# Performance work log

Measured on AMD Instinct MI355X. Metric: run time of the kernel, lower is better.

The kernel has to match this reference:

```python
import jax, jax.numpy as jnp
import numpy as np

RATIO = 4

def positional_encoding(d_model, max_len, w_s):
    # w_s: (B,) per-example frequency warp. pe[b, p, 0::2]=sin, pe[b, p, 1::2]=cos
    pos = jnp.arange(max_len, dtype=jnp.float32)                      # (L,)
    div = jnp.power(10000.0, jnp.arange(0, d_model, 2, dtype=jnp.float32) / d_model)  # (d/2,)
    ang = w_s[:, None, None] * pos[None, :, None] / div[None, None, :]  # (B, L, d/2)
    pe = jnp.stack([jnp.sin(ang), jnp.cos(ang)], axis=-1)             # (B, L, d/2, 2)
    return pe.reshape(w_s.shape[0], max_len, d_model)

def setup_inputs() -> dict:
    key = jax.random.key(0)
    ks = jax.random.split(key, 6)
    B, Tds, L, D = 32, 2048, 512, 256
    q = jax.random.normal(ks[0], (B, Tds, D), dtype=jnp.float32)
    k = jax.random.normal(ks[1], (B, L, D), dtype=jnp.float32)
    v = jax.random.normal(ks[2], (B, L, D), dtype=jnp.float32)
    w_compress = jax.random.normal(ks[3], (D // RATIO, D), dtype=jnp.float32) * (D ** -0.5)
    text_lengths = jax.random.randint(ks[4], (B,), L // 2, L + 1).at[0].set(L)
    mel_lengths = jax.random.randint(ks[5], (B,), (Tds * RATIO) // 2, Tds * RATIO + 1).at[0].set(Tds * RATIO)
    return {"q": q, "k": k, "v": v, "w_compress": w_compress,
            "text_lengths": text_lengths, "mel_lengths": mel_lengths}

def reference(q, k, v, w_compress, text_lengths, mel_lengths):
    B, Tds, D = q.shape
    L = k.shape[1]
    # padding masks (True = padded)
    text_mask = jnp.arange(L)[None, :] >= text_lengths[:, None]            # (B, L)
    mel_mask_ds = jnp.arange(Tds)[None, :] >= (mel_lengths // RATIO)[:, None]  # (B, Tds)
    # positional encodings
    q = q + positional_encoding(D, Tds, jnp.ones((B,), dtype=jnp.float32))
    w_s = mel_lengths.astype(jnp.float32) / RATIO / text_lengths.astype(jnp.float32)
    k = k + positional_encoding(D, L, w_s)
    q = q * (float(D) ** -0.5)
    # scores + masked softmax over text axis
    scores = jnp.einsum('btd,bld->btl', q, k)                              # (B, Tds, L)
    scores = jnp.where(text_mask[:, None, :], -jnp.inf, scores)
    align = jax.nn.softmax(scores, axis=-1)
    align = jnp.where(mel_mask_ds[:, :, None], 0.0, align)
    # hard argmax one-hot, straight-through blend
    idx = jnp.argmax(align, axis=-1)                                       # (B, Tds)
    align_oh = jax.nn.one_hot(idx, L, dtype=align.dtype)
    align_oh = jnp.where(mel_mask_ds[:, :, None], 0.0, align_oh)
    blend = align + jax.lax.stop_gradient(align_oh - align)
    attn = jnp.einsum('btl,bld->btd', blend, v)                            # (B, Tds, D)
    # Compress (Linear D -> D//ratio, no bias) then transpose(1,2)
    out = jnp.einsum('btd,cd->bct', attn, w_compress)                      # (B, D//ratio, Tds)
    return out, align
```

## Files before the change

kernel.cpp:

```cpp
#include <hip/hip_runtime.h>
#include <math.h>

#define NB  32
#define TDS 2048
#define LL  512
#define DD  256
#define DC  64
#define GAP_THR 4e-4f

typedef __attribute__((ext_vector_type(8)))  short short8;
typedef __attribute__((ext_vector_type(16))) float f32x16;

__device__ __forceinline__ unsigned short f2bf(float x) {
    union { float f; unsigned u; } v; v.f = x;
    unsigned r = v.u + 0x7fffu + ((v.u >> 16) & 1u);
    return (unsigned short)(r >> 16);
}
__device__ __forceinline__ float bf2f(unsigned short h) {
    union { unsigned u; float f; } v; v.u = ((unsigned)h) << 16;
    return v.f;
}


__global__ void peq_kernel(float* __restrict__ peq, int* __restrict__ cnt) {
    int idx = blockIdx.x * 256 + threadIdx.x;
    if (idx == 0) cnt[0] = 0;
    int t = idx >> 8;
    int d = idx & 255;
    int i = d >> 1;
    double invdiv = exp((double)i * (-9.210340371976184 / 128.0));
    double ang = (double)t * invdiv;
    double s, c;
    sincos(ang, &s, &c);
    peq[idx] = (float)((d & 1) ? c : s);
}

__global__ __launch_bounds__(256)
void pek_kernel(const float* __restrict__ k,
                const int* __restrict__ text_lengths,
                const int* __restrict__ mel_lengths,
                char* __restrict__ kps) {
    __shared__ double invdiv[128];
    const int tid = threadIdx.x;
    if (tid < 128) invdiv[tid] = exp((double)tid * (-9.210340371976184 / 128.0));
    __syncthreads();
    int f = blockIdx.x * 256 + tid;
    int b = f >> 14;
    int r = f & 16383;
    int ks = r >> 11;
    int r2 = r & 2047;
    int cs = r2 >> 7;
    int r3 = r2 & 127;
    int kh = r3 >> 6;
    int g  = (r3 >> 5) & 1;
    int lane32 = r3 & 31;
    int l  = cs * 32 + lane32;
    int k0 = ks * 32 + kh * 16 + g * 8;
    const float* kr = k + ((size_t)(b * LL + l)) * DD + k0;
    float4 kv0 = *(const float4*)(kr);
    float4 kv1 = *(const float4*)(kr + 4);
    float kv[8] = {kv0.x, kv0.y, kv0.z, kv0.w, kv1.x, kv1.y, kv1.z, kv1.w};
    double wsd = ((double)mel_lengths[b] * 0.25) / (double)text_lengths[b];
    double base_ang = wsd * (double)l;
    unsigned short h[8], lo8[8];
#pragma unroll
    for (int jj = 0; jj < 4; ++jj) {
        int i = (k0 >> 1) + jj;
        double ang = base_ang * invdiv[i];
        double n = rint(ang * 0.15915494309189535);
        double red = fma(n, -6.283185307179586, ang);
        float sn, cs2;
        sincosf((float)red, &sn, &cs2);
        float e0 = kv[2 * jj] + sn;
        float e1 = kv[2 * jj + 1] + cs2;
        h[2 * jj]       = f2bf(e0);
        h[2 * jj + 1]   = f2bf(e1);
        lo8[2 * jj]     = f2bf(e0 - bf2f(h[2 * jj]));
        lo8[2 * jj + 1] = f2bf(e1 - bf2f(h[2 * jj + 1]));
    }
    size_t off = (size_t)b * 524288 + (size_t)ks * 65536 + (size_t)cs * 4096
               + kh * 1024 + g * 512 + lane32 * 16;
    uint4 hv, lv;
    hv.x = h[0] | ((unsigned)h[1] << 16); hv.y = h[2] | ((unsigned)h[3] << 16);
    hv.z = h[4] | ((unsigned)h[5] << 16); hv.w = h[6] | ((unsigned)h[7] << 16);
    lv.x = lo8[0] | ((unsigned)lo8[1] << 16); lv.y = lo8[2] | ((unsigned)lo8[3] << 16);
    lv.z = lo8[4] | ((unsigned)lo8[5] << 16); lv.w = lo8[6] | ((unsigned)lo8[7] << 16);
    *(uint4*)(kps + off) = hv;
    *(uint4*)(kps + off + 2048) = lv;
}

__global__ __launch_bounds__(256, 3)
void score_kernel(const float* __restrict__ q,
                  const float* __restrict__ peq,
                  const char* __restrict__ kps,
                  const int* __restrict__ text_lengths,
                  const int* __restrict__ mel_lengths,
                  float* __restrict__ align_out,
                  int* __restrict__ idx_out,
                  int* __restrict__ flag_cnt,
                  int* __restrict__ flags) {
    __shared__ alignas(16) char smA[32768];
    struct Epi {
        float v1[4][32]; int i1[4][32]; float v2[4][32];
        float S[4][32];  float M[32];
    };
    __shared__ Epi ep;

    const int wgid = blockIdx.x;
    const int xcd = wgid & 7, loc = wgid >> 3;
    const int nid = xcd * 256 + loc;
    const int b  = nid >> 6;
    const int t0 = (nid & 63) << 5;

    const int tid = threadIdx.x;
    const int wn = tid >> 6, lane = tid & 63;
    const int c31 = lane & 31, hi5 = lane >> 5;
    const int tlen = text_lengths[b];
    const int melq = mel_lengths[b] >> 2;

    const char* kpb = kps + (size_t)b * 524288 + (size_t)(hi5 * 512 + c31 * 16);

    f32x16 acc[4];
#pragma unroll
    for (int ci = 0; ci < 4; ++ci)
#pragma unroll
        for (int rg = 0; rg < 16; ++rg) acc[ci][rg] = 0.f;

#define BLOAD(dst, ksv, civ)                                                    \
    {                                                                           \
        const char* p_ = kpb + (ksv) * 65536 + (wn * 4 + (civ)) * 4096;         \
        (dst)[0] = *(const short8*)(p_);                                        \
        (dst)[1] = *(const short8*)(p_ + 1024);                                 \
        (dst)[2] = *(const short8*)(p_ + 2048);                                 \
        (dst)[3] = *(const short8*)(p_ + 3072);                                 \
    }
#define MFMA6(CI, B)                                                            \
    {                                                                           \
        acc[CI] = __builtin_amdgcn_mfma_f32_32x32x16_bf16(ah0, (B)[0], acc[CI], 0, 0, 0); \
        acc[CI] = __builtin_amdgcn_mfma_f32_32x32x16_bf16(ah0, (B)[2], acc[CI], 0, 0, 0); \
        acc[CI] = __builtin_amdgcn_mfma_f32_32x32x16_bf16(al0, (B)[0], acc[CI], 0, 0, 0); \
        acc[CI] = __builtin_amdgcn_mfma_f32_32x32x16_bf16(ah1, (B)[1], acc[CI], 0, 0, 0); \
        acc[CI] = __builtin_amdgcn_mfma_f32_32x32x16_bf16(ah1, (B)[3], acc[CI], 0, 0, 0); \
        acc[CI] = __builtin_amdgcn_mfma_f32_32x32x16_bf16(al1, (B)[1], acc[CI], 0, 0, 0); \
    }

    short8 Bs[3][4];
    BLOAD(Bs[0], 0, 0)
    BLOAD(Bs[1], 0, 1)

    {
        const int sr = tid >> 3, kc = tid & 7;
        const float* qr = q   + ((size_t)(b * TDS) + t0 + sr) * DD;
        const float* pr = peq + (size_t)(t0 + sr) * DD;
#pragma unroll
        for (int kq = 0; kq < 4; ++kq) {
            int m = kq * 8 + kc;
            int k0 = m * 8;
            float4 qa = *(const float4*)(qr + k0);
            float4 qb4 = *(const float4*)(qr + k0 + 4);
            float4 pa = *(const float4*)(pr + k0);
            float4 pb = *(const float4*)(pr + k0 + 4);
            float e[8] = {(qa.x + pa.x) * 0.0625f, (qa.y + pa.y) * 0.0625f,
                          (qa.z + pa.z) * 0.0625f, (qa.w + pa.w) * 0.0625f,
                          (qb4.x + pb.x) * 0.0625f, (qb4.y + pb.y) * 0.0625f,
                          (qb4.z + pb.z) * 0.0625f, (qb4.w + pb.w) * 0.0625f};
            unsigned short h[8], lo[8];
#pragma unroll
            for (int j = 0; j < 8; ++j) {
                h[j] = f2bf(e[j]);
                lo[j] = f2bf(e[j] - bf2f(h[j]));
            }
            uint4 hv, lv;
            hv.x = h[0] | ((unsigned)h[1] << 16); hv.y = h[2] | ((unsigned)h[3] << 16);
            hv.z = h[4] | ((unsigned)h[5] << 16); hv.w = h[6] | ((unsigned)h[7] << 16);
            lv.x = lo[0] | ((unsigned)lo[1] << 16); lv.y = lo[2] | ((unsigned)lo[3] << 16);
            lv.z = lo[4] | ((unsigned)lo[5] << 16); lv.w = lo[6] | ((unsigned)lo[7] << 16);
            int base = (m >> 2) * 4096 + ((m >> 1) & 1) * 1024 + (m & 1) * 512 + sr * 16;
            *(uint4*)(smA + base) = hv;
            *(uint4*)(smA + base + 2048) = lv;
        }
    }
    __syncthreads();

    const int afr = hi5 * 512 + c31 * 16;
    short8 ah0, ah1, al0, al1;
#pragma unroll
    for (int p = 0; p < 32; ++p) {
        if ((p & 3) == 0) {
            const char* ab = smA + (p >> 2) * 4096 + afr;
            ah0 = *(const short8*)(ab);
            ah1 = *(const short8*)(ab + 1024);
            al0 = *(const short8*)(ab + 2048);
            al1 = *(const short8*)(ab + 3072);
        }
        if (p + 2 < 32) BLOAD(Bs[(p + 2) % 3], (p + 2) >> 2, (p + 2) & 3)
        MFMA6(p & 3, Bs[p % 3])
    }
#undef BLOAD
#undef MFMA6

    const float NEGINF = -__builtin_inff();
#pragma unroll
    for (int ci = 0; ci < 4; ++ci) {
        int col = wn * 128 + ci * 32 + c31;
        if (col >= tlen) {
#pragma unroll
            for (int rg = 0; rg < 16; ++rg) acc[ci][rg] = NEGINF;
        }
    }
    float v1[16]; int i1[16]; float v2[16];
#pragma unroll
    for (int rg = 0; rg < 16; ++rg) {
        v1[rg] = acc[0][rg]; i1[rg] = wn * 128 + c31; v2[rg] = NEGINF;
#pragma unroll
        for (int ci = 1; ci < 4; ++ci) {
            float v = acc[ci][rg]; int col = wn * 128 + ci * 32 + c31;
            if (v > v1[rg]) { v2[rg] = v1[rg]; v1[rg] = v; i1[rg] = col; }
            else if (v > v2[rg]) v2[rg] = v;
        }
    }
#pragma unroll
    for (int off = 1; off <= 16; off <<= 1) {
#pragma unroll
        for (int rg = 0; rg < 16; ++rg) {
            float ov1 = __shfl_xor(v1[rg], off, 64);
            int   oi1 = __shfl_xor(i1[rg], off, 64);
            float ov2 = __shfl_xor(v2[rg], off, 64);
            if (ov1 > v1[rg]) { v2[rg] = fmaxf(v1[rg], ov2); v1[rg] = ov1; i1[rg] = oi1; }
            else if (ov1 < v1[rg]) { v2[rg] = fmaxf(v2[rg], ov1); }
            else { i1[rg] = min(i1[rg], oi1); v2[rg] = v1[rg]; }
        }
    }
    if (c31 == 0) {
#pragma unroll
        for (int rg = 0; rg < 16; ++rg) {
            int r32 = (rg & 3) + 8 * (rg >> 2) + 4 * hi5;
            ep.v1[wn][r32] = v1[rg]; ep.i1[wn][r32] = i1[rg]; ep.v2[wn][r32] = v2[rg];
        }
    }
    __syncthreads();
    {
        const int r32 = c31;
        float V1 = ep.v1[0][r32]; int I1 = ep.i1[0][r32]; float V2 = ep.v2[0][r32];
#pragma unroll
        for (int w = 1; w < 4; ++w) {
            float cv1 = ep.v1[w][r32]; int ci1 = ep.i1[w][r32]; float cv2 = ep.v2[w][r32];
            if (cv1 > V1) { V2 = fmaxf(V1, cv2); V1 = cv1; I1 = ci1; }
            else if (cv1 < V1) { V2 = fmaxf(V2, cv1); }
            else { V2 = V1; }
        }
        if (wn == 0 && hi5 == 0) {
            int t = t0 + r32;
            idx_out[b * TDS + t] = I1;
            if (t < melq && (V1 - V2) < GAP_THR) {
                int pos = atomicAdd(flag_cnt, 1);
                flags[pos] = (b << 11) | t;
            }
            ep.M[r32] = V1;
        }
    }
    __syncthreads();
    float ssum[16];
#pragma unroll
    for (int rg = 0; rg < 16; ++rg) {
        int r32 = (rg & 3) + 8 * (rg >> 2) + 4 * hi5;
        float M = ep.M[r32];
        float s = 0.f;
#pragma unroll
        for (int ci = 0; ci < 4; ++ci) {
            float p = __expf(acc[ci][rg] - M);
            acc[ci][rg] = p; s += p;
        }
        ssum[rg] = s;
    }
#pragma unroll
    for (int off = 1; off <= 16; off <<= 1)
#pragma unroll
        for (int rg = 0; rg < 16; ++rg) ssum[rg] += __shfl_xor(ssum[rg], off, 64);
    if (c31 == 0) {
#pragma unroll
        for (int rg = 0; rg < 16; ++rg) {
            int r32 = (rg & 3) + 8 * (rg >> 2) + 4 * hi5;
            ep.S[wn][r32] = ssum[rg];
        }
    }
    __syncthreads();
#pragma unroll
    for (int rg = 0; rg < 16; ++rg) {
        int r32 = (rg & 3) + 8 * (rg >> 2) + 4 * hi5;
        int t = t0 + r32;
        float denom = ep.S[0][r32] + ep.S[1][r32] + ep.S[2][r32] + ep.S[3][r32];
        float sc = (t < melq) ? (1.0f / denom) : 0.f;
        size_t obase = ((size_t)(b * TDS + t)) * LL + wn * 128 + c31;
#pragma unroll
        for (int ci = 0; ci < 4; ++ci)
            __builtin_nontemporal_store(acc[ci][rg] * sc, align_out + obase + ci * 32);
    }
}

__global__ __launch_bounds__(256)
void refine_kernel(const float* __restrict__ q,
                   const float* __restrict__ k,
                   const int* __restrict__ text_lengths,
                   const int* __restrict__ mel_lengths,
                   const int* __restrict__ flags,
                   const int* __restrict__ flag_cnt,
                   int* __restrict__ idx_out) {
    __shared__ double qd[DD];
    __shared__ double invdiv[128];
    __shared__ double rbest[4];
    __shared__ int    ribest[4];
    const int tid = threadIdx.x;
    if (tid < 128)
        invdiv[tid] = 1.0 / pow(10000.0, (double)tid * (1.0 / 128.0));
    const int cnt = flag_cnt[0];
    for (int r = blockIdx.x; r < cnt; r += gridDim.x) {
        const int code = flags[r];
        const int b = code >> 11, t = code & 2047;
        const int tlen = text_lengths[b];
        const double ws = ((double)mel_lengths[b] * 0.25) / (double)text_lengths[b];
        __syncthreads();
        {
            const int d = tid, i = d >> 1;
            double ang = (double)t * invdiv[i];
            double sn, cs;
            sincos(ang, &sn, &cs);
            qd[d] = ((double)q[((size_t)b * TDS + t) * DD + d] + ((d & 1) ? cs : sn)) * 0.0625;
        }
        __syncthreads();
        double best = -1.0e300; int bi = 0x7fffffff;
        for (int p = 0; p < 2; ++p) {
            const int l = tid + p * 256;
            if (l < tlen) {
                const float* kr = k + ((size_t)b * LL + l) * DD;
                const double wl = ws * (double)l;
                double sacc = 0.0;
                for (int i = 0; i < 128; ++i) {
                    double ang = wl * invdiv[i];
                    double sn, cs;
                    sincos(ang, &sn, &cs);
                    sacc += ((double)kr[2 * i]     + sn) * qd[2 * i];
                    sacc += ((double)kr[2 * i + 1] + cs) * qd[2 * i + 1];
                }
                if (sacc > best || (sacc == best && l < bi)) { best = sacc; bi = l; }
            }
        }
        for (int off = 1; off <= 32; off <<= 1) {
            double ov = __shfl_xor(best, off, 64);
            int   oi = __shfl_xor(bi, off, 64);
            if (ov > best || (ov == best && oi < bi)) { best = ov; bi = oi; }
        }
        const int wv = tid >> 6;
        if ((tid & 63) == 0) { rbest[wv] = best; ribest[wv] = bi; }
        __syncthreads();
        if (tid == 0) {
            double bb = rbest[0]; int ii = ribest[0];
            for (int w = 1; w < 4; ++w)
                if (rbest[w] > bb || (rbest[w] == bb && ribest[w] < ii)) { bb = rbest[w]; ii = ribest[w]; }
            idx_out[b * TDS + t] = ii;
        }
    }
}

__global__ __launch_bounds__(256)
void compress_kernel(const float* __restrict__ v,
                     const float* __restrict__ wc,
                     const int* __restrict__ idx_in,
                     const int* __restrict__ mel_lengths,
                     float* __restrict__ out) {
    __shared__ float Ws[16 * 68];
    __shared__ float Vs[16 * 68];
    __shared__ int   idxs[64];
    const int b   = blockIdx.y;
    const int t0  = blockIdx.x * 64;
    const int tid = threadIdx.x;
    const int melq = mel_lengths[b] >> 2;
    const float* vb = v + (size_t)b * LL * DD;

    if (tid < 64) {
        int t = t0 + tid;
        int ii = idx_in[b * TDS + t];
        idxs[tid] = (t >= melq) ? -1 : ii;
    }

    const int tx = tid >> 5;
    const int ty = tid & 31;
    const int sc = tid >> 2;
    const int su = tid & 3;
    float acc[8][2];
#pragma unroll
    for (int i = 0; i < 8; ++i) { acc[i][0] = 0.f; acc[i][1] = 0.f; }

    for (int ks = 0; ks < 16; ++ks) {
        const int d0 = ks * 16;
        __syncthreads();
        {
            float4 wv = *(const float4*)(wc + (size_t)sc * DD + d0 + su * 4);
            Ws[(su * 4 + 0) * 68 + sc] = wv.x;
            Ws[(su * 4 + 1) * 68 + sc] = wv.y;
            Ws[(su * 4 + 2) * 68 + sc] = wv.z;
            Ws[(su * 4 + 3) * 68 + sc] = wv.w;
            int row = idxs[sc];
            float4 vv = make_float4(0.f, 0.f, 0.f, 0.f);
            if (row >= 0) vv = *(const float4*)(vb + (size_t)row * DD + d0 + su * 4);
            Vs[(su * 4 + 0) * 68 + sc] = vv.x;
            Vs[(su * 4 + 1) * 68 + sc] = vv.y;
            Vs[(su * 4 + 2) * 68 + sc] = vv.z;
            Vs[(su * 4 + 3) * 68 + sc] = vv.w;
        }
        __syncthreads();
#pragma unroll
        for (int kk = 0; kk < 16; ++kk) {
            const float* wrow = Ws + kk * 68 + tx * 8;
            float4 a0 = *(const float4*)(wrow);
            float4 a1 = *(const float4*)(wrow + 4);
            float2 bb = *(const float2*)(Vs + kk * 68 + ty * 2);
            const float av[8] = {a0.x, a0.y, a0.z, a0.w, a1.x, a1.y, a1.z, a1.w};
#pragma unroll
            for (int i = 0; i < 8; ++i) {
                acc[i][0] = fmaf(av[i], bb.x, acc[i][0]);
                acc[i][1] = fmaf(av[i], bb.y, acc[i][1]);
            }
        }
    }
#pragma unroll
    for (int i = 0; i < 8; ++i) {
        int c = tx * 8 + i;
        float2 o = make_float2(acc[i][0], acc[i][1]);
        *(float2*)(out + ((size_t)(b * DC + c)) * TDS + t0 + ty * 2) = o;
    }
}

extern "C" void kernel_launch(void* const* d_in, const int* in_sizes, int n_in,
                              void* d_out, int out_size, void* d_ws, size_t ws_size,
                              hipStream_t stream) {
    const float* q    = (const float*)d_in[0];
    const float* k    = (const float*)d_in[1];
    const float* v    = (const float*)d_in[2];
    const float* wc   = (const float*)d_in[3];
    const int*   text = (const int*)d_in[4];
    const int*   mel  = (const int*)d_in[5];

    float* out   = (float*)d_out;
    float* align = out + (size_t)NB * DC * TDS;

    char*  wsb = (char*)d_ws;
    char*  KPS = wsb;
    float* PEQ = (float*)(wsb + 16777216);
    int*   IDX = (int*)(wsb + 16777216 + 2097152);
    int*   CNT = IDX + (size_t)NB * TDS;
    int*   FLG = CNT + 1;

    hipLaunchKernelGGL(peq_kernel, dim3(TDS * DD / 256), dim3(256), 0, stream, PEQ, CNT);
    hipLaunchKernelGGL(pek_kernel, dim3(NB * 16384 / 256), dim3(256), 0, stream,
                       k, text, mel, KPS);
    hipLaunchKernelGGL(score_kernel, dim3(2048), dim3(256), 0, stream,
                       q, PEQ, KPS, text, mel, align, IDX, CNT, FLG);
    hipLaunchKernelGGL(refine_kernel, dim3(256), dim3(256), 0, stream,
                       q, k, text, mel, FLG, CNT, IDX);
    hipLaunchKernelGGL(compress_kernel, dim3(TDS / 64, NB), dim3(256), 0, stream,
                       v, wc, IDX, mel, out);
}
```

Measured before the change: 215.6 us.

## Merge PE table kernels into one launch and use float sincos in refine

Combines the query positional-encoding table kernel and the key PE/bf16 split kernel into a single launch, using block index ranges to pick the job, which removes one kernel launch and its serialization gap. The refine kernel's inner loop now does double-precision range reduction followed by float sincosf instead of full double sincos, cutting expensive FP64 transcendental work on flagged rows. The change lowers the precision of the PE terms in refine, which could alter near-tie argmax decisions.

```diff
diff --git a/kernel.cpp b/kernel.cpp
--- a/kernel.cpp
+++ b/kernel.cpp
@@ -20,31 +20,38 @@
     union { unsigned u; float f; } v; v.u = ((unsigned)h) << 16;
     return v.f;
 }
-
-
-__global__ void peq_kernel(float* __restrict__ peq, int* __restrict__ cnt) {
-    int idx = blockIdx.x * 256 + threadIdx.x;
-    if (idx == 0) cnt[0] = 0;
-    int t = idx >> 8;
-    int d = idx & 255;
-    int i = d >> 1;
-    double invdiv = exp((double)i * (-9.210340371976184 / 128.0));
-    double ang = (double)t * invdiv;
-    double s, c;
-    sincos(ang, &s, &c);
-    peq[idx] = (float)((d & 1) ? c : s);
-}
+__device__ __forceinline__ void rr_sincosf(double ang, float* s, float* c) {
+    double n = rint(ang * 0.15915494309189535);
+    double red = fma(n, -6.283185307179586, ang);
+    sincosf((float)red, s, c);
+}
+
 
 __global__ __launch_bounds__(256)
-void pek_kernel(const float* __restrict__ k,
-                const int* __restrict__ text_lengths,
-                const int* __restrict__ mel_lengths,
-                char* __restrict__ kps) {
+void tables_kernel(const float* __restrict__ k,
+                   const int* __restrict__ text_lengths,
+                   const int* __restrict__ mel_lengths,
+                   float* __restrict__ peq,
+                   char* __restrict__ kps,
+                   int* __restrict__ cnt) {
+    const int tid = threadIdx.x;
+    if (blockIdx.x < 2048) {
+        int idx = blockIdx.x * 256 + tid;
+        if (idx == 0) cnt[0] = 0;
+        int t = idx >> 8;
+        int d = idx & 255;
+        int i = d >> 1;
+        double invd = exp((double)i * (-9.210340371976184 / 128.0));
+        double ang = (double)t * invd;
+        double s, c;
+        sincos(ang, &s, &c);
+        peq[idx] = (float)((d & 1) ? c : s);
+        return;
+    }
     __shared__ double invdiv[128];
-    const int tid = threadIdx.x;
     if (tid < 128) invdiv[tid] = exp((double)tid * (-9.210340371976184 / 128.0));
     __syncthreads();
-    int f = blockIdx.x * 256 + tid;
+    int f = (blockIdx.x - 2048) * 256 + tid;
     int b = f >> 14;
     int r = f & 16383;
     int ks = r >> 11;
@@ -66,11 +73,8 @@
 #pragma unroll
     for (int jj = 0; jj < 4; ++jj) {
         int i = (k0 >> 1) + jj;
-        double ang = base_ang * invdiv[i];
-        double n = rint(ang * 0.15915494309189535);
-        double red = fma(n, -6.283185307179586, ang);
         float sn, cs2;
-        sincosf((float)red, &sn, &cs2);
+        rr_sincosf(base_ang * invdiv[i], &sn, &cs2);
         float e0 = kv[2 * jj] + sn;
         float e1 = kv[2 * jj + 1] + cs2;
         h[2 * jj]       = f2bf(e0);
@@ -322,10 +326,10 @@
         __syncthreads();
         {
             const int d = tid, i = d >> 1;
-            double ang = (double)t * invdiv[i];
-            double sn, cs;
-            sincos(ang, &sn, &cs);
-            qd[d] = ((double)q[((size_t)b * TDS + t) * DD + d] + ((d & 1) ? cs : sn)) * 0.0625;
+            float sn, cs;
+            rr_sincosf((double)t * invdiv[i], &sn, &cs);
+            qd[d] = ((double)q[((size_t)b * TDS + t) * DD + d]
+                     + (double)((d & 1) ? cs : sn)) * 0.0625;
         }
         __syncthreads();
         double best = -1.0e300; int bi = 0x7fffffff;
@@ -336,11 +340,10 @@
                 const double wl = ws * (double)l;
                 double sacc = 0.0;
                 for (int i = 0; i < 128; ++i) {
-                    double ang = wl * invdiv[i];
-                    double sn, cs;
-                    sincos(ang, &sn, &cs);
-                    sacc += ((double)kr[2 * i]     + sn) * qd[2 * i];
-                    sacc += ((double)kr[2 * i + 1] + cs) * qd[2 * i + 1];
+                    float sn, cs;
+                    rr_sincosf(wl * invdiv[i], &sn, &cs);
+                    sacc += ((double)kr[2 * i]     + (double)sn) * qd[2 * i];
+                    sacc += ((double)kr[2 * i + 1] + (double)cs) * qd[2 * i + 1];
                 }
                 if (sacc > best || (sacc == best && l < bi)) { best = sacc; bi = l; }
             }
@@ -451,9 +454,8 @@
     int*   CNT = IDX + (size_t)NB * TDS;
     int*   FLG = CNT + 1;
 
-    hipLaunchKernelGGL(peq_kernel, dim3(TDS * DD / 256), dim3(256), 0, stream, PEQ, CNT);
-    hipLaunchKernelGGL(pek_kernel, dim3(NB * 16384 / 256), dim3(256), 0, stream,
-                       k, text, mel, KPS);
+    hipLaunchKernelGGL(tables_kernel, dim3(4096), dim3(256), 0, stream,
+                       k, text, mel, PEQ, KPS, CNT);
     hipLaunchKernelGGL(score_kernel, dim3(2048), dim3(256), 0, stream,
                        q, PEQ, KPS, text, mel, align, IDX, CNT, FLG);
     hipLaunchKernelGGL(refine_kernel, dim3(256), dim3(256), 0, stream,
```

Result: faster. 199.5 us (-7.5%).
